# Performance work log

Measured on AMD Instinct MI355X. Metric: run time of the kernel, lower is better.

## Reference

```python
import jax, jax.numpy as jnp
import numpy as np

D = 512
T = 64
MID_GROUPS = 8
EPS = 1e-5


def _scorer(x, W1, b1, W2, b2):
    # nn.Linear(D, D//2) -> GELU (exact erf) -> nn.Linear(D//2, 1)
    h = jax.nn.gelu(x @ W1 + b1, approximate=False)
    return h @ W2 + b2  # [..., 1]


def setup_inputs() -> dict:
    key = jax.random.key(0)
    ks = jax.random.split(key, 16)
    B = 1024
    x = jax.random.normal(ks[0], (B, T, D), dtype=jnp.float32)
    inp = {"x": x}
    # three per-scale attention scorers
    for i in range(3):
        s1 = 1.0 / np.sqrt(D)
        s2 = 1.0 / np.sqrt(D // 2)
        inp[f"W1_{i}"] = jax.random.uniform(ks[1 + 4 * i], (D, D // 2), jnp.float32, -s1, s1)
        inp[f"b1_{i}"] = jax.random.uniform(ks[2 + 4 * i], (D // 2,), jnp.float32, -s1, s1)
        inp[f"W2_{i}"] = jax.random.uniform(ks[3 + 4 * i], (D // 2, 1), jnp.float32, -s2, s2)
        inp[f"b2_{i}"] = jax.random.uniform(ks[4 + 4 * i], (1,), jnp.float32, -s2, s2)
    sp = 1.0 / np.sqrt(3 * D)
    inp["Wp"] = jax.random.uniform(ks[13], (3 * D, D), jnp.float32, -sp, sp)
    inp["bp"] = jax.random.uniform(ks[14], (D,), jnp.float32, -sp, sp)
    inp["ln_g"] = jnp.ones((D,), jnp.float32)
    inp["ln_b"] = jnp.zeros((D,), jnp.float32)
    return inp


def reference(x, W1_0, b1_0, W2_0, b2_0, W1_1, b1_1, W2_1, b2_1,
              W1_2, b1_2, W2_2, b2_2, Wp, bp, ln_g, ln_b):
    B, Tn, Dn = x.shape

    # --- scale 0: global pool (n_groups == 1), softmax over all T ---
    s0 = _scorer(x, W1_0, b1_0, W2_0, b2_0)          # [B,T,1]
    w0 = jax.nn.softmax(s0, axis=1)
    pooled0 = jnp.sum(x * w0, axis=1, keepdims=True)  # [B,1,D]
    scale0 = jnp.broadcast_to(pooled0, (B, Tn, Dn))

    # --- scale 1: MID_GROUPS even groups, softmax within each group ---
    S = Tn // MID_GROUPS
    xg = x.reshape(B, MID_GROUPS, S, Dn)
    s1 = _scorer(xg, W1_1, b1_1, W2_1, b2_1)          # [B,G,S,1]
    w1 = jax.nn.softmax(s1, axis=2)
    pooled1 = jnp.sum(xg * w1, axis=2, keepdims=True) # [B,G,1,D]
    scale1 = jnp.broadcast_to(pooled1, (B, MID_GROUPS, S, Dn)).reshape(B, Tn, Dn)

    # --- scale 2: per-segment (n_groups == T), sigmoid gate ---
    s2 = _scorer(x, W1_2, b1_2, W2_2, b2_2)           # [B,T,1]
    scale2 = x * jax.nn.sigmoid(s2)

    multi = jnp.concatenate([scale0, scale1, scale2], axis=-1)  # [B,T,3D]
    h = jax.nn.gelu(multi @ Wp + bp, approximate=False)
    mu = jnp.mean(h, axis=-1, keepdims=True)
    var = jnp.mean((h - mu) ** 2, axis=-1, keepdims=True)
    out = (h - mu) * jax.lax.rsqrt(var + EPS) * ln_g + ln_b
    return out  # dropout is identity in eval mode
```

## Files before the change

### kernel.cpp

```cpp
#include <hip/hip_runtime.h>
#include <hip/hip_bf16.h>

typedef __attribute__((ext_vector_type(8))) short short8;
typedef __attribute__((ext_vector_type(4))) float f32x4;

#define BT 65536
#define D  512
#define NB 1024
#define NH 768

static __device__ __forceinline__ unsigned short f2bf(float f) {
    union { __hip_bfloat16 h; unsigned short u; } cv;
    cv.h = __float2bfloat16(f);
    return cv.u;
}

static __device__ __forceinline__ float gelu(float x) {
    return 0.5f * x * (1.0f + erff(x * 0.70710678118654752f));
}

static __device__ __forceinline__ int swz(int row, int ch) {
    return row * 128 + (((ch ^ (row & 7)) & 7) << 4);
}

__global__ void convert_x(const float* __restrict__ x, unsigned short* __restrict__ xb) {
    size_t i = ((size_t)blockIdx.x * 256 + threadIdx.x) * 4;
    float4 v = *(const float4*)(x + i);
    ushort4 o;
    o.x = f2bf(v.x); o.y = f2bf(v.y); o.z = f2bf(v.z); o.w = f2bf(v.w);
    *(ushort4*)(xb + i) = o;
}

__global__ void transpose_to_bf16(const float* __restrict__ in, unsigned short* __restrict__ out,
                                  int R, int C, int ostride) {
    __shared__ float tile[32][33];
    int r0 = blockIdx.x * 32, c0 = blockIdx.y * 32;
    int tx = threadIdx.x, ty = threadIdx.y;
    for (int yy = 0; yy < 32; yy += 8)
        tile[ty + yy][tx] = in[(size_t)(r0 + ty + yy) * C + c0 + tx];
    __syncthreads();
    for (int yy = 0; yy < 32; yy += 8)
        out[(size_t)(c0 + ty + yy) * ostride + r0 + tx] = f2bf(tile[tx][ty + yy]);
}

__global__ void prep_cat(const float* b1_0, const float* b1_1, const float* b1_2,
                         const float* W2_0, const float* W2_1, const float* W2_2,
                         const float* b2_0, const float* b2_1, const float* b2_2,
                         float* b1cat, float* W2cat, float* b2cat) {
    int t = threadIdx.x;
    int s = t >> 8, j = t & 255;
    const float* b1p = (s == 0) ? b1_0 : (s == 1) ? b1_1 : b1_2;
    const float* w2p = (s == 0) ? W2_0 : (s == 1) ? W2_1 : W2_2;
    b1cat[t] = b1p[j];
    W2cat[t] = w2p[j];
    if (t < 3) b2cat[t] = (t == 0 ? b2_0 : t == 1 ? b2_1 : b2_2)[0];
}

__global__ __launch_bounds__(512) void scorer_gemm(
        const unsigned short* __restrict__ xb, const unsigned short* __restrict__ W1T,
        const float* __restrict__ b1cat, const float* __restrict__ W2cat,
        const float* __restrict__ b2cat, float* __restrict__ s_out) {
    __shared__ char ldsA[64 * 128];
    __shared__ char ldsB[256 * 128];
    __shared__ float red[64 * 4];
    int tid = threadIdx.x, lane = tid & 63, w = tid >> 6;
    int wr = w >> 2, wc = w & 3;
    int sc = blockIdx.y;
    size_t rowbase = (size_t)blockIdx.x * 64;
    const unsigned short* Wt = W1T + (size_t)sc * 256 * 512;
    f32x4 acc[2][4] = {};
    for (int kt = 0; kt < 8; ++kt) {
        int k0 = kt * 64;
        __syncthreads();
        { int r = tid >> 3, ch = tid & 7;
          *(int4*)(ldsA + swz(r, ch)) = *(const int4*)(xb + (rowbase + r) * 512 + k0 + ch * 8); }
        for (int i = 0; i < 4; ++i) {
            int idx = i * 512 + tid; int r = idx >> 3, ch = idx & 7;
            *(int4*)(ldsB + swz(r, ch)) = *(const int4*)(Wt + (size_t)r * 512 + k0 + ch * 8);
        }
        __syncthreads();
        for (int kk = 0; kk < 2; ++kk) {
            int chunk = kk * 4 + (lane >> 4);
            short8 af[2], bfr[4];
            #pragma unroll
            for (int m = 0; m < 2; ++m)
                af[m] = *(const short8*)(ldsA + swz(wr * 32 + m * 16 + (lane & 15), chunk));
            #pragma unroll
            for (int n = 0; n < 4; ++n)
                bfr[n] = *(const short8*)(ldsB + swz(wc * 64 + n * 16 + (lane & 15), chunk));
            #pragma unroll
            for (int m = 0; m < 2; ++m)
                #pragma unroll
                for (int n = 0; n < 4; ++n)
                    acc[m][n] = __builtin_amdgcn_mfma_f32_16x16x32_bf16(af[m], bfr[n], acc[m][n], 0, 0, 0);
        }
    }
    float b1v[4], w2v[4];
    #pragma unroll
    for (int n = 0; n < 4; ++n) {
        int col = wc * 64 + n * 16 + (lane & 15);
        b1v[n] = b1cat[sc * 256 + col];
        w2v[n] = W2cat[sc * 256 + col];
    }
    #pragma unroll
    for (int m = 0; m < 2; ++m)
        #pragma unroll
        for (int j = 0; j < 4; ++j) {
            float p = 0.f;
            #pragma unroll
            for (int n = 0; n < 4; ++n)
                p += gelu(acc[m][n][j] + b1v[n]) * w2v[n];
            for (int off = 1; off < 16; off <<= 1) p += __shfl_xor(p, off);
            if ((lane & 15) == 0)
                red[(wr * 32 + m * 16 + (lane >> 4) * 4 + j) * 4 + wc] = p;
        }
    __syncthreads();
    if (tid < 64) {
        float sv = red[tid * 4] + red[tid * 4 + 1] + red[tid * 4 + 2] + red[tid * 4 + 3] + b2cat[sc];
        s_out[(size_t)sc * BT + rowbase + tid] = sv;
    }
}

__global__ __launch_bounds__(256) void pool_kernel(
        const float* __restrict__ x, const float* __restrict__ s_all,
        unsigned short* __restrict__ pooledcat, unsigned short* __restrict__ gx) {
    __shared__ float w0s[64], w1s[64], gts[64];
    int tid = threadIdx.x;
    size_t b = blockIdx.x;
    int w = tid >> 6, lane = tid & 63;
    if (w == 0) {
        float v = s_all[b * 64 + lane];
        float m = v;
        for (int off = 32; off; off >>= 1) m = fmaxf(m, __shfl_xor(m, off));
        float e = expf(v - m);
        float su = e;
        for (int off = 32; off; off >>= 1) su += __shfl_xor(su, off);
        w0s[lane] = e / su;
    } else if (w == 1) {
        float v = s_all[BT + b * 64 + lane];
        float m = v;
        for (int off = 4; off; off >>= 1) m = fmaxf(m, __shfl_xor(m, off));
        float e = expf(v - m);
        float su = e;
        for (int off = 4; off; off >>= 1) su += __shfl_xor(su, off);
        w1s[lane] = e / su;
    } else if (w == 2) {
        float v = s_all[2 * BT + b * 64 + lane];
        gts[lane] = 1.0f / (1.0f + expf(-v));
    }
    __syncthreads();
    for (int half = 0; half < 2; ++half) {
        int c = tid + half * 256;
        float a0 = 0.f, a1 = 0.f;
        #pragma unroll 8
        for (int t = 0; t < 64; ++t) {
            float xv = x[(b * 64 + t) * 512 + c];
            a0 += w0s[t] * xv;
            a1 += w1s[t] * xv;
            gx[(b * 64 + t) * 512 + c] = f2bf(xv * gts[t]);
            if ((t & 7) == 7) {
                pooledcat[(b * 8 + (t >> 3)) * 1024 + 512 + c] = f2bf(a1);
                a1 = 0.f;
            }
        }
        unsigned short p0 = f2bf(a0);
        for (int g = 0; g < 8; ++g) pooledcat[(b * 8 + g) * 1024 + c] = p0;
    }
}

__global__ __launch_bounds__(256) void base_gemm(
        const unsigned short* __restrict__ pooledcat, const unsigned short* __restrict__ WpT,
        const float* __restrict__ bp, float* __restrict__ baseout) {
    __shared__ char ldsA[32 * 128];
    __shared__ char ldsB[512 * 128];
    int tid = threadIdx.x, lane = tid & 63, w = tid >> 6;
    size_t rowbase = (size_t)blockIdx.x * 32;
    f32x4 acc[2][8] = {};
    for (int kt = 0; kt < 16; ++kt) {
        int k0 = kt * 64;
        __syncthreads();
        { int r = tid >> 3, ch = tid & 7;
          *(int4*)(ldsA + swz(r, ch)) = *(const int4*)(pooledcat + (rowbase + r) * 1024 + k0 + ch * 8); }
        for (int i = 0; i < 16; ++i) {
            int idx = i * 256 + tid; int r = idx >> 3, ch = idx & 7;
            *(int4*)(ldsB + swz(r, ch)) = *(const int4*)(WpT + (size_t)r * 1536 + k0 + ch * 8);
        }
        __syncthreads();
        for (int kk = 0; kk < 2; ++kk) {
            int chunk = kk * 4 + (lane >> 4);
            short8 af[2], bfr[8];
            #pragma unroll
            for (int m = 0; m < 2; ++m)
                af[m] = *(const short8*)(ldsA + swz(m * 16 + (lane & 15), chunk));
            #pragma unroll
            for (int n = 0; n < 8; ++n)
                bfr[n] = *(const short8*)(ldsB + swz(w * 128 + n * 16 + (lane & 15), chunk));
            #pragma unroll
            for (int m = 0; m < 2; ++m)
                #pragma unroll
                for (int n = 0; n < 8; ++n)
                    acc[m][n] = __builtin_amdgcn_mfma_f32_16x16x32_bf16(af[m], bfr[n], acc[m][n], 0, 0, 0);
        }
    }
    #pragma unroll
    for (int n = 0; n < 8; ++n) {
        int col = w * 128 + n * 16 + (lane & 15);
        float bpv = bp[col];
        #pragma unroll
        for (int m = 0; m < 2; ++m)
            #pragma unroll
            for (int j = 0; j < 4; ++j) {
                int row = m * 16 + (lane >> 4) * 4 + j;
                baseout[(rowbase + row) * 512 + col] = acc[m][n][j] + bpv;
            }
    }
}

__global__ __launch_bounds__(512) void final_gemm_ln(
        const unsigned short* __restrict__ gx, const unsigned short* __restrict__ WpT,
        const float* __restrict__ base, const float* __restrict__ ln_g,
        const float* __restrict__ ln_b, float* __restrict__ out) {
    __shared__ char ldsA[64 * 128];
    __shared__ char ldsB[512 * 128];
    __shared__ float redS[64][4], redQ[64][4], muL[64], rsL[64];
    int tid = threadIdx.x, lane = tid & 63, w = tid >> 6;
    int wr = w >> 2, wc = w & 3;
    size_t b = blockIdx.x;
    size_t rowbase = b * 64;
    f32x4 acc[2][8] = {};
    for (int kt = 0; kt < 8; ++kt) {
        int k0 = kt * 64;
        __syncthreads();
        { int r = tid >> 3, ch = tid & 7;
          *(int4*)(ldsA + swz(r, ch)) = *(const int4*)(gx + (rowbase + r) * 512 + k0 + ch * 8); }
        for (int i = 0; i < 8; ++i) {
            int idx = i * 512 + tid; int r = idx >> 3, ch = idx & 7;
            *(int4*)(ldsB + swz(r, ch)) = *(const int4*)(WpT + (size_t)r * 1536 + 1024 + k0 + ch * 8);
        }
        __syncthreads();
        for (int kk = 0; kk < 2; ++kk) {
            int chunk = kk * 4 + (lane >> 4);
            short8 af[2], bfr[8];
            #pragma unroll
            for (int m = 0; m < 2; ++m)
                af[m] = *(const short8*)(ldsA + swz(wr * 32 + m * 16 + (lane & 15), chunk));
            #pragma unroll
            for (int n = 0; n < 8; ++n)
                bfr[n] = *(const short8*)(ldsB + swz(wc * 128 + n * 16 + (lane & 15), chunk));
            #pragma unroll
            for (int m = 0; m < 2; ++m)
                #pragma unroll
                for (int n = 0; n < 8; ++n)
                    acc[m][n] = __builtin_amdgcn_mfma_f32_16x16x32_bf16(af[m], bfr[n], acc[m][n], 0, 0, 0);
        }
    }
    float lngv[8], lnbv[8];
    int cols[8];
    #pragma unroll
    for (int n = 0; n < 8; ++n) {
        int col = wc * 128 + n * 16 + (lane & 15);
        cols[n] = col;
        lngv[n] = ln_g[col];
        lnbv[n] = ln_b[col];
    }
    #pragma unroll
    for (int m = 0; m < 2; ++m) {
        int gi = wr * 4 + m * 2 + ((lane >> 4) >> 1);
        #pragma unroll
        for (int n = 0; n < 8; ++n) {
            float bv = base[(b * 8 + gi) * 512 + cols[n]];
            #pragma unroll
            for (int j = 0; j < 4; ++j)
                acc[m][n][j] = gelu(acc[m][n][j] + bv);
        }
    }
    #pragma unroll
    for (int m = 0; m < 2; ++m)
        #pragma unroll
        for (int j = 0; j < 4; ++j) {
            float s = 0.f, q = 0.f;
            #pragma unroll
            for (int n = 0; n < 8; ++n) { float v = acc[m][n][j]; s += v; q += v * v; }
            for (int off = 1; off < 16; off <<= 1) { s += __shfl_xor(s, off); q += __shfl_xor(q, off); }
            if ((lane & 15) == 0) {
                int row = wr * 32 + m * 16 + (lane >> 4) * 4 + j;
                redS[row][wc] = s;
                redQ[row][wc] = q;
            }
        }
    __syncthreads();
    if (tid < 64) {
        float s = redS[tid][0] + redS[tid][1] + redS[tid][2] + redS[tid][3];
        float q = redQ[tid][0] + redQ[tid][1] + redQ[tid][2] + redQ[tid][3];
        float mu = s * (1.0f / 512.0f);
        float var = q * (1.0f / 512.0f) - mu * mu;
        muL[tid] = mu;
        rsL[tid] = rsqrtf(var + 1e-5f);
    }
    __syncthreads();
    #pragma unroll
    for (int m = 0; m < 2; ++m)
        #pragma unroll
        for (int j = 0; j < 4; ++j) {
            int row = wr * 32 + m * 16 + (lane >> 4) * 4 + j;
            float mu = muL[row], rs = rsL[row];
            #pragma unroll
            for (int n = 0; n < 8; ++n)
                out[(rowbase + row) * 512 + cols[n]] = (acc[m][n][j] - mu) * rs * lngv[n] + lnbv[n];
        }
}

extern "C" void kernel_launch(void* const* d_in, const int* in_sizes, int n_in,
                              void* d_out, int out_size, void* d_ws, size_t ws_size,
                              hipStream_t stream) {
    const float* x    = (const float*)d_in[0];
    const float* W1a[3] = { (const float*)d_in[1], (const float*)d_in[5], (const float*)d_in[9] };
    const float* b1a[3] = { (const float*)d_in[2], (const float*)d_in[6], (const float*)d_in[10] };
    const float* W2a[3] = { (const float*)d_in[3], (const float*)d_in[7], (const float*)d_in[11] };
    const float* b2a[3] = { (const float*)d_in[4], (const float*)d_in[8], (const float*)d_in[12] };
    const float* Wp   = (const float*)d_in[13];
    const float* bp   = (const float*)d_in[14];
    const float* ln_g = (const float*)d_in[15];
    const float* ln_b = (const float*)d_in[16];
    float* out = (float*)d_out;

    char* ws = (char*)d_ws;
    size_t off = 0;
    auto carve = [&](size_t bytes) { char* p = ws + off; off += (bytes + 255) & ~(size_t)255; return p; };
    unsigned short* xb        = (unsigned short*)carve((size_t)BT * D * 2);
    unsigned short* gx        = xb;
    unsigned short* W1T       = (unsigned short*)carve((size_t)NH * D * 2);
    unsigned short* WpT       = (unsigned short*)carve((size_t)D * 1536 * 2);
    float*          b1cat     = (float*)carve(NH * 4);
    float*          W2cat     = (float*)carve(NH * 4);
    float*          b2cat     = (float*)carve(16);
    float*          s_all     = (float*)carve((size_t)3 * BT * 4);
    unsigned short* pooledcat = (unsigned short*)carve((size_t)NB * 8 * 1024 * 2);
    float*          base      = (float*)carve((size_t)NB * 8 * 512 * 4);

    convert_x<<<32768, 256, 0, stream>>>(x, xb);
    dim3 tb(32, 8);
    for (int s = 0; s < 3; ++s)
        transpose_to_bf16<<<dim3(16, 8), tb, 0, stream>>>(W1a[s], W1T + (size_t)s * 256 * 512, 512, 256, 512);
    transpose_to_bf16<<<dim3(48, 16), tb, 0, stream>>>(Wp, WpT, 1536, 512, 1536);
    prep_cat<<<1, 768, 0, stream>>>(b1a[0], b1a[1], b1a[2], W2a[0], W2a[1], W2a[2],
                                    b2a[0], b2a[1], b2a[2], b1cat, W2cat, b2cat);
    scorer_gemm<<<dim3(1024, 3), 512, 0, stream>>>(xb, W1T, b1cat, W2cat, b2cat, s_all);
    pool_kernel<<<1024, 256, 0, stream>>>(x, s_all, pooledcat, gx);
    base_gemm<<<256, 256, 0, stream>>>(pooledcat, WpT, bp, base);
    final_gemm_ln<<<1024, 512, 0, stream>>>(gx, WpT, base, ln_g, ln_b, out);
}
```

Before: 532.6 us.

## Fuse bf16 conversion, scorers and pooling into one kernel; enlarge final GEMM tile

Removes the separate x-to-bf16 conversion pass and merges the three-scale scorer GEMM with the softmax/sigmoid pooling into a single per-batch kernel. The block now reads fp32 x directly, converts it on the fly into LDS, and computes all 768 hidden columns at once, so the scores never go through global memory and x is re-read only once for pooling. The final GEMM+LayerNorm now processes 128 rows per block instead of 64. In exchange, LDS use per block is much larger (about 100KB for the weight tile) and there are more accumulator registers, which lowers occupancy.

```diff
diff --git a/kernel.cpp b/kernel.cpp
--- a/kernel.cpp
+++ b/kernel.cpp
@@ -23,12 +23,13 @@
     return row * 128 + (((ch ^ (row & 7)) & 7) << 4);
 }
 
-__global__ void convert_x(const float* __restrict__ x, unsigned short* __restrict__ xb) {
-    size_t i = ((size_t)blockIdx.x * 256 + threadIdx.x) * 4;
-    float4 v = *(const float4*)(x + i);
-    ushort4 o;
-    o.x = f2bf(v.x); o.y = f2bf(v.y); o.z = f2bf(v.z); o.w = f2bf(v.w);
-    *(ushort4*)(xb + i) = o;
+static __device__ __forceinline__ short8 pack8(const float4& v0, const float4& v1) {
+    short8 r;
+    r[0] = (short)f2bf(v0.x); r[1] = (short)f2bf(v0.y);
+    r[2] = (short)f2bf(v0.z); r[3] = (short)f2bf(v0.w);
+    r[4] = (short)f2bf(v1.x); r[5] = (short)f2bf(v1.y);
+    r[6] = (short)f2bf(v1.z); r[7] = (short)f2bf(v1.w);
+    return r;
 }
 
 __global__ void transpose_to_bf16(const float* __restrict__ in, unsigned short* __restrict__ out,
@@ -56,115 +57,146 @@
     if (t < 3) b2cat[t] = (t == 0 ? b2_0 : t == 1 ? b2_1 : b2_2)[0];
 }
 
-__global__ __launch_bounds__(512) void scorer_gemm(
-        const unsigned short* __restrict__ xb, const unsigned short* __restrict__ W1T,
+__global__ __launch_bounds__(512) void scorer_pool(
+        const float* __restrict__ x, const unsigned short* __restrict__ W1T,
         const float* __restrict__ b1cat, const float* __restrict__ W2cat,
-        const float* __restrict__ b2cat, float* __restrict__ s_out) {
+        const float* __restrict__ b2cat,
+        unsigned short* __restrict__ pooledcat, unsigned short* __restrict__ gx) {
     __shared__ char ldsA[64 * 128];
-    __shared__ char ldsB[256 * 128];
-    __shared__ float red[64 * 4];
-    int tid = threadIdx.x, lane = tid & 63, w = tid >> 6;
-    int wr = w >> 2, wc = w & 3;
-    int sc = blockIdx.y;
-    size_t rowbase = (size_t)blockIdx.x * 64;
-    const unsigned short* Wt = W1T + (size_t)sc * 256 * 512;
-    f32x4 acc[2][4] = {};
+    __shared__ char ldsB[768 * 128];
+    __shared__ float red[3][64][8];
+    __shared__ float sarr[3][64];
+    __shared__ float w0s[64], w1s[64], gts[64];
+    __shared__ float a0p[4][512];
+    int tid = threadIdx.x, lane = tid & 63, wid = tid >> 6;
+    size_t b = blockIdx.x;
+    size_t rowbase = b * 64;
+    f32x4 acc[4][6] = {};
     for (int kt = 0; kt < 8; ++kt) {
         int k0 = kt * 64;
         __syncthreads();
         { int r = tid >> 3, ch = tid & 7;
-          *(int4*)(ldsA + swz(r, ch)) = *(const int4*)(xb + (rowbase + r) * 512 + k0 + ch * 8); }
-        for (int i = 0; i < 4; ++i) {
+          const float* src = x + (rowbase + r) * 512 + k0 + ch * 8;
+          float4 v0 = *(const float4*)src;
+          float4 v1 = *(const float4*)(src + 4);
+          *(short8*)(ldsA + swz(r, ch)) = pack8(v0, v1); }
+        #pragma unroll
+        for (int i = 0; i < 12; ++i) {
             int idx = i * 512 + tid; int r = idx >> 3, ch = idx & 7;
-            *(int4*)(ldsB + swz(r, ch)) = *(const int4*)(Wt + (size_t)r * 512 + k0 + ch * 8);
-        }
-        __syncthreads();
+            *(short8*)(ldsB + swz(r, ch)) = *(const short8*)(W1T + (size_t)r * 512 + k0 + ch * 8);
+        }
+        __syncthreads();
+        #pragma unroll
         for (int kk = 0; kk < 2; ++kk) {
             int chunk = kk * 4 + (lane >> 4);
-            short8 af[2], bfr[4];
-            #pragma unroll
-            for (int m = 0; m < 2; ++m)
-                af[m] = *(const short8*)(ldsA + swz(wr * 32 + m * 16 + (lane & 15), chunk));
-            #pragma unroll
-            for (int n = 0; n < 4; ++n)
-                bfr[n] = *(const short8*)(ldsB + swz(wc * 64 + n * 16 + (lane & 15), chunk));
-            #pragma unroll
-            for (int m = 0; m < 2; ++m)
+            short8 af[4], bfr[6];
+            #pragma unroll
+            for (int m = 0; m < 4; ++m)
+                af[m] = *(const short8*)(ldsA + swz(m * 16 + (lane & 15), chunk));
+            #pragma unroll
+            for (int n = 0; n < 6; ++n)
+                bfr[n] = *(const short8*)(ldsB + swz(wid * 96 + n * 16 + (lane & 15), chunk));
+            #pragma unroll
+            for (int m = 0; m < 4; ++m)
                 #pragma unroll
-                for (int n = 0; n < 4; ++n)
+                for (int n = 0; n < 6; ++n)
                     acc[m][n] = __builtin_amdgcn_mfma_f32_16x16x32_bf16(af[m], bfr[n], acc[m][n], 0, 0, 0);
         }
     }
-    float b1v[4], w2v[4];
-    #pragma unroll
-    for (int n = 0; n < 4; ++n) {
-        int col = wc * 64 + n * 16 + (lane & 15);
-        b1v[n] = b1cat[sc * 256 + col];
-        w2v[n] = W2cat[sc * 256 + col];
-    }
-    #pragma unroll
-    for (int m = 0; m < 2; ++m)
+    float b1v[6], w2v[6];
+    #pragma unroll
+    for (int n = 0; n < 6; ++n) {
+        int col = wid * 96 + n * 16 + (lane & 15);
+        b1v[n] = b1cat[col];
+        w2v[n] = W2cat[col];
+    }
+    int lo = (wid * 96) >> 8, hi = (wid * 96 + 80) >> 8;
+    #pragma unroll
+    for (int m = 0; m < 4; ++m)
         #pragma unroll
         for (int j = 0; j < 4; ++j) {
-            float p = 0.f;
-            #pragma unroll
-            for (int n = 0; n < 4; ++n)
-                p += gelu(acc[m][n][j] + b1v[n]) * w2v[n];
-            for (int off = 1; off < 16; off <<= 1) p += __shfl_xor(p, off);
-            if ((lane & 15) == 0)
-                red[(wr * 32 + m * 16 + (lane >> 4) * 4 + j) * 4 + wc] = p;
-        }
-    __syncthreads();
-    if (tid < 64) {
-        float sv = red[tid * 4] + red[tid * 4 + 1] + red[tid * 4 + 2] + red[tid * 4 + 3] + b2cat[sc];
-        s_out[(size_t)sc * BT + rowbase + tid] = sv;
-    }
-}
-
-__global__ __launch_bounds__(256) void pool_kernel(
-        const float* __restrict__ x, const float* __restrict__ s_all,
-        unsigned short* __restrict__ pooledcat, unsigned short* __restrict__ gx) {
-    __shared__ float w0s[64], w1s[64], gts[64];
-    int tid = threadIdx.x;
-    size_t b = blockIdx.x;
-    int w = tid >> 6, lane = tid & 63;
-    if (w == 0) {
-        float v = s_all[b * 64 + lane];
+            float p0 = 0.f, p1 = 0.f, p2 = 0.f;
+            #pragma unroll
+            for (int n = 0; n < 6; ++n) {
+                float g = gelu(acc[m][n][j] + b1v[n]) * w2v[n];
+                int sc = (wid * 96 + n * 16) >> 8;
+                if (sc == 0) p0 += g; else if (sc == 1) p1 += g; else p2 += g;
+            }
+            if (lo <= 0 && 0 <= hi) for (int off = 1; off < 16; off <<= 1) p0 += __shfl_xor(p0, off);
+            if (lo <= 1 && 1 <= hi) for (int off = 1; off < 16; off <<= 1) p1 += __shfl_xor(p1, off);
+            if (lo <= 2 && 2 <= hi) for (int off = 1; off < 16; off <<= 1) p2 += __shfl_xor(p2, off);
+            if ((lane & 15) == 0) {
+                int row = m * 16 + (lane >> 4) * 4 + j;
+                red[0][row][wid] = p0;
+                red[1][row][wid] = p1;
+                red[2][row][wid] = p2;
+            }
+        }
+    __syncthreads();
+    if (tid < 192) {
+        int sc = tid >> 6, row = tid & 63;
+        float s = b2cat[sc];
+        #pragma unroll
+        for (int k = 0; k < 8; ++k) s += red[sc][row][k];
+        sarr[sc][row] = s;
+    }
+    __syncthreads();
+    if (wid == 0) {
+        float v = sarr[0][lane];
         float m = v;
         for (int off = 32; off; off >>= 1) m = fmaxf(m, __shfl_xor(m, off));
         float e = expf(v - m);
         float su = e;
         for (int off = 32; off; off >>= 1) su += __shfl_xor(su, off);
         w0s[lane] = e / su;
-    } else if (w == 1) {
-        float v = s_all[BT + b * 64 + lane];
+    } else if (wid == 1) {
+        float v = sarr[1][lane];
         float m = v;
         for (int off = 4; off; off >>= 1) m = fmaxf(m, __shfl_xor(m, off));
         float e = expf(v - m);
         float su = e;
         for (int off = 4; off; off >>= 1) su += __shfl_xor(su, off);
         w1s[lane] = e / su;
-    } else if (w == 2) {
-        float v = s_all[2 * BT + b * 64 + lane];
-        gts[lane] = 1.0f / (1.0f + expf(-v));
-    }
-    __syncthreads();
-    for (int half = 0; half < 2; ++half) {
-        int c = tid + half * 256;
-        float a0 = 0.f, a1 = 0.f;
-        #pragma unroll 8
-        for (int t = 0; t < 64; ++t) {
-            float xv = x[(b * 64 + t) * 512 + c];
-            a0 += w0s[t] * xv;
-            a1 += w1s[t] * xv;
-            gx[(b * 64 + t) * 512 + c] = f2bf(xv * gts[t]);
+    } else if (wid == 2) {
+        gts[lane] = 1.0f / (1.0f + expf(-sarr[2][lane]));
+    }
+    __syncthreads();
+    {
+        int c4 = (tid & 127) * 4;
+        int tg = tid >> 7;
+        float a0[4] = {0.f, 0.f, 0.f, 0.f};
+        float a1[4] = {0.f, 0.f, 0.f, 0.f};
+        for (int t = tg * 16; t < tg * 16 + 16; ++t) {
+            float4 xv = *(const float4*)(x + (rowbase + t) * 512 + c4);
+            float wg0 = w0s[t], wg1 = w1s[t], gt = gts[t];
+            a0[0] += wg0 * xv.x; a0[1] += wg0 * xv.y; a0[2] += wg0 * xv.z; a0[3] += wg0 * xv.w;
+            a1[0] += wg1 * xv.x; a1[1] += wg1 * xv.y; a1[2] += wg1 * xv.z; a1[3] += wg1 * xv.w;
+            ushort4 gv;
+            gv.x = f2bf(xv.x * gt); gv.y = f2bf(xv.y * gt);
+            gv.z = f2bf(xv.z * gt); gv.w = f2bf(xv.w * gt);
+            *(ushort4*)(gx + (rowbase + t) * 512 + c4) = gv;
             if ((t & 7) == 7) {
-                pooledcat[(b * 8 + (t >> 3)) * 1024 + 512 + c] = f2bf(a1);
-                a1 = 0.f;
-            }
-        }
-        unsigned short p0 = f2bf(a0);
-        for (int g = 0; g < 8; ++g) pooledcat[(b * 8 + g) * 1024 + c] = p0;
+                ushort4 pv;
+                pv.x = f2bf(a1[0]); pv.y = f2bf(a1[1]); pv.z = f2bf(a1[2]); pv.w = f2bf(a1[3]);
+                *(ushort4*)(pooledcat + (b * 8 + (t >> 3)) * 1024 + 512 + c4) = pv;
+                a1[0] = a1[1] = a1[2] = a1[3] = 0.f;
+            }
+        }
+        #pragma unroll
+        for (int k = 0; k < 4; ++k) a0p[tg][c4 + k] = a0[k];
+    }
+    __syncthreads();
+    if (tid < 128) {
+        int c4 = tid * 4;
+        ushort4 pv;
+        float s0 = a0p[0][c4]     + a0p[1][c4]     + a0p[2][c4]     + a0p[3][c4];
+        float s1 = a0p[0][c4 + 1] + a0p[1][c4 + 1] + a0p[2][c4 + 1] + a0p[3][c4 + 1];
+        float s2 = a0p[0][c4 + 2] + a0p[1][c4 + 2] + a0p[2][c4 + 2] + a0p[3][c4 + 2];
+        float s3 = a0p[0][c4 + 3] + a0p[1][c4 + 3] + a0p[2][c4 + 3] + a0p[3][c4 + 3];
+        pv.x = f2bf(s0); pv.y = f2bf(s1); pv.z = f2bf(s2); pv.w = f2bf(s3);
+        #pragma unroll
+        for (int g = 0; g < 8; ++g)
+            *(ushort4*)(pooledcat + (b * 8 + g) * 1024 + c4) = pv;
     }
 }
 
@@ -220,35 +252,40 @@
         const unsigned short* __restrict__ gx, const unsigned short* __restrict__ WpT,
         const float* __restrict__ base, const float* __restrict__ ln_g,
         const float* __restrict__ ln_b, float* __restrict__ out) {
-    __shared__ char ldsA[64 * 128];
+    __shared__ char ldsA[128 * 128];
     __shared__ char ldsB[512 * 128];
-    __shared__ float redS[64][4], redQ[64][4], muL[64], rsL[64];
+    __shared__ float redS[128][4], redQ[128][4], muL[128], rsL[128];
     int tid = threadIdx.x, lane = tid & 63, w = tid >> 6;
     int wr = w >> 2, wc = w & 3;
-    size_t b = blockIdx.x;
-    size_t rowbase = b * 64;
-    f32x4 acc[2][8] = {};
+    size_t rowbase = (size_t)blockIdx.x * 128;
+    size_t b2base = (size_t)blockIdx.x * 2;
+    f32x4 acc[4][8] = {};
     for (int kt = 0; kt < 8; ++kt) {
         int k0 = kt * 64;
         __syncthreads();
-        { int r = tid >> 3, ch = tid & 7;
-          *(int4*)(ldsA + swz(r, ch)) = *(const int4*)(gx + (rowbase + r) * 512 + k0 + ch * 8); }
+        #pragma unroll
+        for (int i = 0; i < 2; ++i) {
+            int idx = i * 512 + tid; int r = idx >> 3, ch = idx & 7;
+            *(int4*)(ldsA + swz(r, ch)) = *(const int4*)(gx + (rowbase + r) * 512 + k0 + ch * 8);
+        }
+        #pragma unroll
         for (int i = 0; i < 8; ++i) {
             int idx = i * 512 + tid; int r = idx >> 3, ch = idx & 7;
             *(int4*)(ldsB + swz(r, ch)) = *(const int4*)(WpT + (size_t)r * 1536 + 1024 + k0 + ch * 8);
         }
         __syncthreads();
+        #pragma unroll
         for (int kk = 0; kk < 2; ++kk) {
             int chunk = kk * 4 + (lane >> 4);
-            short8 af[2], bfr[8];
-            #pragma unroll
-            for (int m = 0; m < 2; ++m)
-                af[m] = *(const short8*)(ldsA + swz(wr * 32 + m * 16 + (lane & 15), chunk));
+            short8 af[4], bfr[8];
+            #pragma unroll
+            for (int m = 0; m < 4; ++m)
+                af[m] = *(const short8*)(ldsA + swz(wr * 64 + m * 16 + (lane & 15), chunk));
             #pragma unroll
             for (int n = 0; n < 8; ++n)
                 bfr[n] = *(const short8*)(ldsB + swz(wc * 128 + n * 16 + (lane & 15), chunk));
             #pragma unroll
-            for (int m = 0; m < 2; ++m)
+            for (int m = 0; m < 4; ++m)
                 #pragma unroll
                 for (int n = 0; n < 8; ++n)
                     acc[m][n] = __builtin_amdgcn_mfma_f32_16x16x32_bf16(af[m], bfr[n], acc[m][n], 0, 0, 0);
@@ -264,18 +301,18 @@
         lnbv[n] = ln_b[col];
     }
     #pragma unroll
-    for (int m = 0; m < 2; ++m) {
-        int gi = wr * 4 + m * 2 + ((lane >> 4) >> 1);
+    for (int m = 0; m < 4; ++m) {
+        int gi = m * 2 + ((lane >> 4) >> 1);
         #pragma unroll
         for (int n = 0; n < 8; ++n) {
-            float bv = base[(b * 8 + gi) * 512 + cols[n]];
+            float bv = base[((b2base + wr) * 8 + gi) * 512 + cols[n]];
             #pragma unroll
             for (int j = 0; j < 4; ++j)
                 acc[m][n][j] = gelu(acc[m][n][j] + bv);
         }
     }
     #pragma unroll
-    for (int m = 0; m < 2; ++m)
+    for (int m = 0; m < 4; ++m)
         #pragma unroll
         for (int j = 0; j < 4; ++j) {
             float s = 0.f, q = 0.f;
@@ -283,13 +320,13 @@
             for (int n = 0; n < 8; ++n) { float v = acc[m][n][j]; s += v; q += v * v; }
             for (int off = 1; off < 16; off <<= 1) { s += __shfl_xor(s, off); q += __shfl_xor(q, off); }
             if ((lane & 15) == 0) {
-                int row = wr * 32 + m * 16 + (lane >> 4) * 4 + j;
+                int row = wr * 64 + m * 16 + (lane >> 4) * 4 + j;
                 redS[row][wc] = s;
                 redQ[row][wc] = q;
             }
         }
     __syncthreads();
-    if (tid < 64) {
+    if (tid < 128) {
         float s = redS[tid][0] + redS[tid][1] + redS[tid][2] + redS[tid][3];
         float q = redQ[tid][0] + redQ[tid][1] + redQ[tid][2] + redQ[tid][3];
         float mu = s * (1.0f / 512.0f);
@@ -299,10 +336,10 @@
     }
     __syncthreads();
     #pragma unroll
-    for (int m = 0; m < 2; ++m)
+    for (int m = 0; m < 4; ++m)
         #pragma unroll
         for (int j = 0; j < 4; ++j) {
-            int row = wr * 32 + m * 16 + (lane >> 4) * 4 + j;
+            int row = wr * 64 + m * 16 + (lane >> 4) * 4 + j;
             float mu = muL[row], rs = rsL[row];
             #pragma unroll
             for (int n = 0; n < 8; ++n)
@@ -327,26 +364,22 @@
     char* ws = (char*)d_ws;
     size_t off = 0;
     auto carve = [&](size_t bytes) { char* p = ws + off; off += (bytes + 255) & ~(size_t)255; return p; };
-    unsigned short* xb        = (unsigned short*)carve((size_t)BT * D * 2);
-    unsigned short* gx        = xb;
+    unsigned short* gx        = (unsigned short*)carve((size_t)BT * D * 2);
     unsigned short* W1T       = (unsigned short*)carve((size_t)NH * D * 2);
     unsigned short* WpT       = (unsigned short*)carve((size_t)D * 1536 * 2);
     float*          b1cat     = (float*)carve(NH * 4);
     float*          W2cat     = (float*)carve(NH * 4);
     float*          b2cat     = (float*)carve(16);
-    float*          s_all     = (float*)carve((size_t)3 * BT * 4);
     unsigned short* pooledcat = (unsigned short*)carve((size_t)NB * 8 * 1024 * 2);
     float*          base      = (float*)carve((size_t)NB * 8 * 512 * 4);
 
-    convert_x<<<32768, 256, 0, stream>>>(x, xb);
     dim3 tb(32, 8);
     for (int s = 0; s < 3; ++s)
         transpose_to_bf16<<<dim3(16, 8), tb, 0, stream>>>(W1a[s], W1T + (size_t)s * 256 * 512, 512, 256, 512);
     transpose_to_bf16<<<dim3(48, 16), tb, 0, stream>>>(Wp, WpT, 1536, 512, 1536);
     prep_cat<<<1, 768, 0, stream>>>(b1a[0], b1a[1], b1a[2], W2a[0], W2a[1], W2a[2],
                                     b2a[0], b2a[1], b2a[2], b1cat, W2cat, b2cat);
-    scorer_gemm<<<dim3(1024, 3), 512, 0, stream>>>(xb, W1T, b1cat, W2cat, b2cat, s_all);
-    pool_kernel<<<1024, 256, 0, stream>>>(x, s_all, pooledcat, gx);
+    scorer_pool<<<1024, 512, 0, stream>>>(x, W1T, b1cat, W2cat, b2cat, pooledcat, gx);
     base_gemm<<<256, 256, 0, stream>>>(pooledcat, WpT, bp, base);
-    final_gemm_ln<<<1024, 512, 0, stream>>>(gx, WpT, base, ln_g, ln_b, out);
-}
+    final_gemm_ln<<<512, 512, 0, stream>>>(gx, WpT, base, ln_g, ln_b, out);
+}
```

After: 597.3 us. +12.1%, slower.
